# Kernel optimization log

Measured on AMD Instinct MI355X. Metric: run time of the kernel, lower is better.

The kernel has to match this reference:

```python
import jax, jax.numpy as jnp
import numpy as np

N_NODES = 100000
N_EDGES = 2000000
D_IN = 4
HID = 64


def setup_inputs() -> dict:
    key = jax.random.key(0)
    ks = jax.random.split(key, 8)
    node_feats = jax.random.normal(ks[0], (N_NODES, D_IN), dtype=jnp.float32)
    pairs = jax.random.randint(ks[1], (N_EDGES, 2), 0, N_NODES, dtype=jnp.int64)
    # Kaiming-ish init scaling
    W1 = jax.random.normal(ks[2], (D_IN, HID), dtype=jnp.float32) / np.sqrt(D_IN)
    b1 = jnp.zeros((HID,), dtype=jnp.float32)
    W2 = jax.random.normal(ks[3], (HID, HID), dtype=jnp.float32) / np.sqrt(HID)
    b2 = jnp.zeros((HID,), dtype=jnp.float32)
    We1 = jax.random.normal(ks[4], (3 * HID, HID), dtype=jnp.float32) / np.sqrt(3 * HID)
    be1 = jnp.zeros((HID,), dtype=jnp.float32)
    We2 = jax.random.normal(ks[5], (HID, 1), dtype=jnp.float32) / np.sqrt(HID)
    be2 = jnp.zeros((1,), dtype=jnp.float32)
    return {"node_feats": node_feats, "pairs": pairs, "W1": W1, "b1": b1,
            "W2": W2, "b2": b2, "We1": We1, "be1": be1, "We2": We2, "be2": be2}


def reference(node_feats, pairs, W1, b1, W2, b2, We1, be1, We2, be2):
    # node MLP: Linear -> ReLU -> Linear -> ReLU
    H = jax.nn.relu(node_feats @ W1 + b1)      # [N, HID]
    H = jax.nn.relu(H @ W2 + b2)               # [N, HID]
    # vectorized gather over all edge pairs (replaces Python loop)
    hu = H[pairs[:, 0]]                        # [E, HID]
    hv = H[pairs[:, 1]]                        # [E, HID]
    E = jnp.concatenate([hu, hv, jnp.abs(hu - hv)], axis=-1)  # [E, 3*HID]
    # edge MLP: Linear -> ReLU -> Linear, squeeze last dim
    scores = (jax.nn.relu(E @ We1 + be1) @ We2 + be2)[:, 0]   # [E]
    return scores
```

## Files before the change

### kernel.cpp

```cpp
#include <hip/hip_runtime.h>

#define N_NODES 100000
#define N_EDGES 2000000

typedef __bf16 bf16x8 __attribute__((ext_vector_type(8)));
typedef float f32x4 __attribute__((ext_vector_type(4)));

__device__ __forceinline__ unsigned f2bf_rne(float f) {
  unsigned u = __builtin_bit_cast(unsigned, f);
  u += 0x7FFFu + ((u >> 16) & 1u);
  return u >> 16;
}

__device__ __forceinline__ unsigned pack_rhu(float lo, float hi) {
  unsigned ulo = __builtin_bit_cast(unsigned, lo) + 0x8000u;
  unsigned uhi = __builtin_bit_cast(unsigned, hi) + 0x8000u;
  return __builtin_amdgcn_perm(uhi, ulo, 0x07060302u);
}

__device__ __forceinline__ unsigned absdiff_pack(unsigned a, unsigned b) {
  float alo = __builtin_bit_cast(float, a << 16);
  float ahi = __builtin_bit_cast(float, a & 0xFFFF0000u);
  float blo = __builtin_bit_cast(float, b << 16);
  float bhi = __builtin_bit_cast(float, b & 0xFFFF0000u);
  return pack_rhu(fabsf(alo - blo), fabsf(ahi - bhi));
}

__global__ __launch_bounds__(64, 1) void node_mfma_kernel(
    const float* __restrict__ X, const float* __restrict__ W1,
    const float* __restrict__ b1, const float* __restrict__ W2,
    const float* __restrict__ b2, unsigned short* __restrict__ H) {
  const int lane = threadIdx.x;
  const int l15 = lane & 15;
  const int quad = lane >> 4;

  float w1v[2][4][8], b1v[2][8];
#pragma unroll
  for (int c = 0; c < 2; ++c)
#pragma unroll
    for (int j = 0; j < 8; ++j) {
      int col = c * 32 + quad * 8 + j;
      b1v[c][j] = b1[col];
#pragma unroll
      for (int d = 0; d < 4; ++d) w1v[c][d][j] = W1[d * 64 + col];
    }

  uint4 afr[2][4];
#pragma unroll
  for (int c = 0; c < 2; ++c)
#pragma unroll
    for (int mt = 0; mt < 4; ++mt) {
      unsigned w[4];
#pragma unroll
      for (int p = 0; p < 4; ++p) {
        int k = c * 32 + quad * 8 + 2 * p;
        unsigned lo = f2bf_rne(W2[k * 64 + mt * 16 + l15]);
        unsigned hi = f2bf_rne(W2[(k + 1) * 64 + mt * 16 + l15]);
        w[p] = lo | (hi << 16);
      }
      afr[c][mt] = make_uint4(w[0], w[1], w[2], w[3]);
    }
  float b2v[16];
#pragma unroll
  for (int mt = 0; mt < 4; ++mt)
#pragma unroll
    for (int r = 0; r < 4; ++r) b2v[mt * 4 + r] = b2[mt * 16 + quad * 4 + r];

  const int ntiles = N_NODES / 16;
  for (int tile = blockIdx.x; tile < ntiles; tile += gridDim.x) {
    float4 xv = ((const float4*)X)[tile * 16 + l15];

    uint4 bfr[2];
#pragma unroll
    for (int c = 0; c < 2; ++c) {
      unsigned w[4];
#pragma unroll
      for (int p = 0; p < 4; ++p) {
        float h0 = fmaxf(b1v[c][2 * p] + xv.x * w1v[c][0][2 * p] +
                             xv.y * w1v[c][1][2 * p] + xv.z * w1v[c][2][2 * p] +
                             xv.w * w1v[c][3][2 * p],
                         0.f);
        float h1 = fmaxf(b1v[c][2 * p + 1] + xv.x * w1v[c][0][2 * p + 1] +
                             xv.y * w1v[c][1][2 * p + 1] +
                             xv.z * w1v[c][2][2 * p + 1] +
                             xv.w * w1v[c][3][2 * p + 1],
                         0.f);
        w[p] = pack_rhu(h0, h1);
      }
      bfr[c] = make_uint4(w[0], w[1], w[2], w[3]);
    }

    f32x4 acc[4];
#pragma unroll
    for (int mt = 0; mt < 4; ++mt) acc[mt] = (f32x4){0.f, 0.f, 0.f, 0.f};
#pragma unroll
    for (int c = 0; c < 2; ++c)
#pragma unroll
      for (int mt = 0; mt < 4; ++mt)
        acc[mt] = __builtin_amdgcn_mfma_f32_16x16x32_bf16(
            __builtin_bit_cast(bf16x8, afr[c][mt]),
            __builtin_bit_cast(bf16x8, bfr[c]), acc[mt], 0, 0, 0);

    unsigned short* hrow = H + (tile * 16 + l15) * 64;
#pragma unroll
    for (int mt = 0; mt < 4; ++mt) {
      unsigned lo = pack_rhu(fmaxf(acc[mt][0] + b2v[mt * 4 + 0], 0.f),
                             fmaxf(acc[mt][1] + b2v[mt * 4 + 1], 0.f));
      unsigned hi = pack_rhu(fmaxf(acc[mt][2] + b2v[mt * 4 + 2], 0.f),
                             fmaxf(acc[mt][3] + b2v[mt * 4 + 3], 0.f));
      *(uint2*)(hrow + mt * 16 + quad * 4) = make_uint2(lo, hi);
    }
  }
}

__global__ __launch_bounds__(256, 2) void edge_mlp_kernel(
    const unsigned short* __restrict__ H, const int* __restrict__ pairs,
    const float* __restrict__ We1, const float* __restrict__ be1,
    const float* __restrict__ We2, const float* __restrict__ be2,
    float* __restrict__ out) {
  const int tid = threadIdx.x;
  const int lane = tid & 63;
  const int l15 = lane & 15;
  const int quad = lane >> 4;

  uint4 afr[6][4];
#pragma unroll
  for (int c = 0; c < 6; ++c)
#pragma unroll
    for (int mt = 0; mt < 4; ++mt) {
      unsigned w[4];
#pragma unroll
      for (int p = 0; p < 4; ++p) {
        int k = c * 32 + quad * 8 + 2 * p;
        unsigned lo = f2bf_rne(We1[k * 64 + mt * 16 + l15]);
        unsigned hi = f2bf_rne(We1[(k + 1) * 64 + mt * 16 + l15]);
        w[p] = lo | (hi << 16);
      }
      afr[c][mt] = make_uint4(w[0], w[1], w[2], w[3]);
    }
  float be1v[16], we2v[16];
#pragma unroll
  for (int mt = 0; mt < 4; ++mt)
#pragma unroll
    for (int r = 0; r < 4; ++r) {
      be1v[mt * 4 + r] = be1[mt * 16 + quad * 4 + r];
      we2v[mt * 4 + r] = We2[mt * 16 + quad * 4 + r];
    }
  const float be2v = be2[0];

  const int wid = blockIdx.x * 4 + (tid >> 6);
  const int nw = gridDim.x * 4;
  const int ntiles = N_EDGES / 16;
  const int last = ntiles - 1;
  const int2* pairs2 = (const int2*)pairs;

  uint4 g[3][4];
  int2 uvn[3];
#pragma unroll
  for (int k = 0; k < 3; ++k) {
    int t = wid + k * nw;
    int2 uv = pairs2[(t <= last ? t : last) * 16 + l15];
    const uint4* pu = (const uint4*)(H + uv.x * 64 + quad * 8);
    const uint4* pv = (const uint4*)(H + uv.y * 64 + quad * 8);
    g[k][0] = pu[0];
    g[k][1] = pu[4];
    g[k][2] = pv[0];
    g[k][3] = pv[4];
    int tn = t + 3 * nw;
    uvn[k] = pairs2[(tn <= last ? tn : last) * 16 + l15];
  }

  for (int base = wid; base < ntiles; base += 3 * nw) {
#pragma unroll
    for (int k = 0; k < 3; ++k) {
      const int t = base + k * nw;

      uint4 ab0, ab1;
      ab0.x = absdiff_pack(g[k][0].x, g[k][2].x);
      ab0.y = absdiff_pack(g[k][0].y, g[k][2].y);
      ab0.z = absdiff_pack(g[k][0].z, g[k][2].z);
      ab0.w = absdiff_pack(g[k][0].w, g[k][2].w);
      ab1.x = absdiff_pack(g[k][1].x, g[k][3].x);
      ab1.y = absdiff_pack(g[k][1].y, g[k][3].y);
      ab1.z = absdiff_pack(g[k][1].z, g[k][3].z);
      ab1.w = absdiff_pack(g[k][1].w, g[k][3].w);

      bf16x8 b[6];
      b[0] = __builtin_bit_cast(bf16x8, g[k][0]);
      b[1] = __builtin_bit_cast(bf16x8, g[k][1]);
      b[2] = __builtin_bit_cast(bf16x8, g[k][2]);
      b[3] = __builtin_bit_cast(bf16x8, g[k][3]);
      b[4] = __builtin_bit_cast(bf16x8, ab0);
      b[5] = __builtin_bit_cast(bf16x8, ab1);

      f32x4 acc[4];
#pragma unroll
      for (int mt = 0; mt < 4; ++mt) acc[mt] = (f32x4){0.f, 0.f, 0.f, 0.f};
#pragma unroll
      for (int c = 0; c < 6; ++c)
#pragma unroll
        for (int mt = 0; mt < 4; ++mt)
          acc[mt] = __builtin_amdgcn_mfma_f32_16x16x32_bf16(
              __builtin_bit_cast(bf16x8, afr[c][mt]), b[c], acc[mt], 0, 0, 0);

      {
        const uint4* qu = (const uint4*)(H + uvn[k].x * 64 + quad * 8);
        const uint4* qv = (const uint4*)(H + uvn[k].y * 64 + quad * 8);
        g[k][0] = qu[0];
        g[k][1] = qu[4];
        g[k][2] = qv[0];
        g[k][3] = qv[4];
        int tn = t + 6 * nw;
        uvn[k] = pairs2[(tn <= last ? tn : last) * 16 + l15];
      }

      float s = 0.f;
#pragma unroll
      for (int mt = 0; mt < 4; ++mt)
#pragma unroll
        for (int r = 0; r < 4; ++r)
          s += fmaxf(acc[mt][r] + be1v[mt * 4 + r], 0.f) * we2v[mt * 4 + r];
      s += __shfl_xor(s, 16);
      s += __shfl_xor(s, 32);
      if (quad == 0 && t <= last) out[t * 16 + l15] = s + be2v;
    }
  }
}

extern "C" void kernel_launch(void* const* d_in, const int* in_sizes, int n_in,
                              void* d_out, int out_size, void* d_ws,
                              size_t ws_size, hipStream_t stream) {
  const float* X = (const float*)d_in[0];
  const int* pairs = (const int*)d_in[1];
  const float* W1 = (const float*)d_in[2];
  const float* b1 = (const float*)d_in[3];
  const float* W2 = (const float*)d_in[4];
  const float* b2 = (const float*)d_in[5];
  const float* We1 = (const float*)d_in[6];
  const float* be1 = (const float*)d_in[7];
  const float* We2 = (const float*)d_in[8];
  const float* be2 = (const float*)d_in[9];
  float* out = (float*)d_out;
  unsigned short* H = (unsigned short*)d_ws;

  node_mfma_kernel<<<1024, 64, 0, stream>>>(X, W1, b1, W2, b2, H);
  edge_mlp_kernel<<<1024, 256, 0, stream>>>(H, pairs, We1, be1, We2, be2, out);
}
```

Before: 168.6 us.

## Switch edge MLP to 32x32x16 MFMA with LDS-resident weights and bias folding

The edge kernel now processes 32 edges per wave tile using 32x32x16 bf16 MFMA instead of 16x16x32. The We1 weight fragments move from registers into shared memory and are read per MFMA. The be1 bias is folded into an extra K chunk paired with a constant-one operand. This is meant to cut MFMA instruction count and register pressure so more gathers stay in flight. In exchange it adds an LDS read per MFMA, does one extra MFMA chunk for the bias, and rounds the bias to bf16.

Measured after the change: 170.9 us. Within noise of the previous version (+1.4%).

```diff
diff --git a/kernel.cpp b/kernel.cpp
--- a/kernel.cpp
+++ b/kernel.cpp
@@ -5,6 +5,7 @@
 
 typedef __bf16 bf16x8 __attribute__((ext_vector_type(8)));
 typedef float f32x4 __attribute__((ext_vector_type(4)));
+typedef float f32x16 __attribute__((ext_vector_type(16)));
 
 __device__ __forceinline__ unsigned f2bf_rne(float f) {
   unsigned u = __builtin_bit_cast(unsigned, f);
@@ -118,111 +119,125 @@
     const float* __restrict__ We1, const float* __restrict__ be1,
     const float* __restrict__ We2, const float* __restrict__ be2,
     float* __restrict__ out) {
+  __shared__ uint4 wlds[26 * 64];
   const int tid = threadIdx.x;
+
+  for (int s = tid; s < 26 * 64; s += 256) {
+    int f = s >> 6, ln = s & 63;
+    int c = f >> 1, mt = f & 1;
+    int col = mt * 32 + (ln & 31);
+    uint4 val;
+    if (c < 12) {
+      int kb = c * 16 + (ln >> 5) * 8;
+      val.x = f2bf_rne(We1[(kb + 0) * 64 + col]) |
+              (f2bf_rne(We1[(kb + 1) * 64 + col]) << 16);
+      val.y = f2bf_rne(We1[(kb + 2) * 64 + col]) |
+              (f2bf_rne(We1[(kb + 3) * 64 + col]) << 16);
+      val.z = f2bf_rne(We1[(kb + 4) * 64 + col]) |
+              (f2bf_rne(We1[(kb + 5) * 64 + col]) << 16);
+      val.w = f2bf_rne(We1[(kb + 6) * 64 + col]) |
+              (f2bf_rne(We1[(kb + 7) * 64 + col]) << 16);
+    } else {
+      val.x = ((ln >> 5) == 0) ? f2bf_rne(be1[col]) : 0u;
+      val.y = 0u;
+      val.z = 0u;
+      val.w = 0u;
+    }
+    wlds[s] = val;
+  }
+
   const int lane = tid & 63;
-  const int l15 = lane & 15;
-  const int quad = lane >> 4;
-
-  uint4 afr[6][4];
-#pragma unroll
-  for (int c = 0; c < 6; ++c)
-#pragma unroll
-    for (int mt = 0; mt < 4; ++mt) {
-      unsigned w[4];
-#pragma unroll
-      for (int p = 0; p < 4; ++p) {
-        int k = c * 32 + quad * 8 + 2 * p;
-        unsigned lo = f2bf_rne(We1[k * 64 + mt * 16 + l15]);
-        unsigned hi = f2bf_rne(We1[(k + 1) * 64 + mt * 16 + l15]);
-        w[p] = lo | (hi << 16);
-      }
-      afr[c][mt] = make_uint4(w[0], w[1], w[2], w[3]);
-    }
-  float be1v[16], we2v[16];
-#pragma unroll
-  for (int mt = 0; mt < 4; ++mt)
-#pragma unroll
-    for (int r = 0; r < 4; ++r) {
-      be1v[mt * 4 + r] = be1[mt * 16 + quad * 4 + r];
-      we2v[mt * 4 + r] = We2[mt * 16 + quad * 4 + r];
-    }
+  const int n = lane & 31;
+  const int half = lane >> 5;
+
+  uint4 b13u = make_uint4((half == 0) ? 0x00003F80u : 0u, 0u, 0u, 0u);
+
+  float we2v[32];
+#pragma unroll
+  for (int mt = 0; mt < 2; ++mt)
+#pragma unroll
+    for (int r = 0; r < 16; ++r)
+      we2v[mt * 16 + r] = We2[mt * 32 + (r & 3) + 8 * (r >> 2) + 4 * half];
   const float be2v = be2[0];
+  __syncthreads();
 
   const int wid = blockIdx.x * 4 + (tid >> 6);
   const int nw = gridDim.x * 4;
-  const int ntiles = N_EDGES / 16;
+  const int ntiles = N_EDGES / 32;
   const int last = ntiles - 1;
   const int2* pairs2 = (const int2*)pairs;
-
-  uint4 g[3][4];
-  int2 uvn[3];
-#pragma unroll
-  for (int k = 0; k < 3; ++k) {
+  const uint4* wf = wlds + lane;
+
+  uint4 g[2][8];
+  int2 uvn[2];
+#pragma unroll
+  for (int k = 0; k < 2; ++k) {
     int t = wid + k * nw;
-    int2 uv = pairs2[(t <= last ? t : last) * 16 + l15];
-    const uint4* pu = (const uint4*)(H + uv.x * 64 + quad * 8);
-    const uint4* pv = (const uint4*)(H + uv.y * 64 + quad * 8);
-    g[k][0] = pu[0];
-    g[k][1] = pu[4];
-    g[k][2] = pv[0];
-    g[k][3] = pv[4];
-    int tn = t + 3 * nw;
-    uvn[k] = pairs2[(tn <= last ? tn : last) * 16 + l15];
-  }
-
-  for (int base = wid; base < ntiles; base += 3 * nw) {
-#pragma unroll
-    for (int k = 0; k < 3; ++k) {
-      const int t = base + k * nw;
-
-      uint4 ab0, ab1;
-      ab0.x = absdiff_pack(g[k][0].x, g[k][2].x);
-      ab0.y = absdiff_pack(g[k][0].y, g[k][2].y);
-      ab0.z = absdiff_pack(g[k][0].z, g[k][2].z);
-      ab0.w = absdiff_pack(g[k][0].w, g[k][2].w);
-      ab1.x = absdiff_pack(g[k][1].x, g[k][3].x);
-      ab1.y = absdiff_pack(g[k][1].y, g[k][3].y);
-      ab1.z = absdiff_pack(g[k][1].z, g[k][3].z);
-      ab1.w = absdiff_pack(g[k][1].w, g[k][3].w);
-
-      bf16x8 b[6];
-      b[0] = __builtin_bit_cast(bf16x8, g[k][0]);
-      b[1] = __builtin_bit_cast(bf16x8, g[k][1]);
-      b[2] = __builtin_bit_cast(bf16x8, g[k][2]);
-      b[3] = __builtin_bit_cast(bf16x8, g[k][3]);
-      b[4] = __builtin_bit_cast(bf16x8, ab0);
-      b[5] = __builtin_bit_cast(bf16x8, ab1);
-
-      f32x4 acc[4];
-#pragma unroll
-      for (int mt = 0; mt < 4; ++mt) acc[mt] = (f32x4){0.f, 0.f, 0.f, 0.f};
-#pragma unroll
-      for (int c = 0; c < 6; ++c)
-#pragma unroll
-        for (int mt = 0; mt < 4; ++mt)
-          acc[mt] = __builtin_amdgcn_mfma_f32_16x16x32_bf16(
-              __builtin_bit_cast(bf16x8, afr[c][mt]), b[c], acc[mt], 0, 0, 0);
+    t = (t <= last) ? t : last;
+    int2 uv = pairs2[t * 32 + n];
+    const uint4* pu = (const uint4*)(H + uv.x * 64 + half * 8);
+    const uint4* pv = (const uint4*)(H + uv.y * 64 + half * 8);
+#pragma unroll
+    for (int c = 0; c < 4; ++c) {
+      g[k][c] = pu[c * 2];
+      g[k][4 + c] = pv[c * 2];
+    }
+    int tn = wid + (k + 2) * nw;
+    tn = (tn <= last) ? tn : last;
+    uvn[k] = pairs2[tn * 32 + n];
+  }
+
+  for (int base = wid; base < ntiles; base += 2 * nw) {
+#pragma unroll
+    for (int k = 0; k < 2; ++k) {
+      int t = base + k * nw;
+      t = (t <= last) ? t : last;
+
+      uint4 ab[4];
+#pragma unroll
+      for (int c = 0; c < 4; ++c) {
+        ab[c].x = absdiff_pack(g[k][c].x, g[k][4 + c].x);
+        ab[c].y = absdiff_pack(g[k][c].y, g[k][4 + c].y);
+        ab[c].z = absdiff_pack(g[k][c].z, g[k][4 + c].z);
+        ab[c].w = absdiff_pack(g[k][c].w, g[k][4 + c].w);
+      }
+
+      f32x16 acc[2];
+      acc[0] = (f32x16)(0.f);
+      acc[1] = (f32x16)(0.f);
+#pragma unroll
+      for (int c = 0; c < 13; ++c) {
+        uint4 bu = (c < 8) ? g[k][c] : (c < 12 ? ab[c - 8] : b13u);
+        bf16x8 b = __builtin_bit_cast(bf16x8, bu);
+#pragma unroll
+        for (int mt = 0; mt < 2; ++mt) {
+          bf16x8 a = __builtin_bit_cast(bf16x8, wf[(c * 2 + mt) * 64]);
+          acc[mt] = __builtin_amdgcn_mfma_f32_32x32x16_bf16(a, b, acc[mt], 0,
+                                                            0, 0);
+        }
+      }
 
       {
-        const uint4* qu = (const uint4*)(H + uvn[k].x * 64 + quad * 8);
-        const uint4* qv = (const uint4*)(H + uvn[k].y * 64 + quad * 8);
-        g[k][0] = qu[0];
-        g[k][1] = qu[4];
-        g[k][2] = qv[0];
-        g[k][3] = qv[4];
-        int tn = t + 6 * nw;
-        uvn[k] = pairs2[(tn <= last ? tn : last) * 16 + l15];
+        const uint4* qu = (const uint4*)(H + uvn[k].x * 64 + half * 8);
+        const uint4* qv = (const uint4*)(H + uvn[k].y * 64 + half * 8);
+#pragma unroll
+        for (int c = 0; c < 4; ++c) {
+          g[k][c] = qu[c * 2];
+          g[k][4 + c] = qv[c * 2];
+        }
+        int tn = base + (k + 4) * nw;
+        tn = (tn <= last) ? tn : last;
+        uvn[k] = pairs2[tn * 32 + n];
       }
 
       float s = 0.f;
 #pragma unroll
-      for (int mt = 0; mt < 4; ++mt)
-#pragma unroll
-        for (int r = 0; r < 4; ++r)
-          s += fmaxf(acc[mt][r] + be1v[mt * 4 + r], 0.f) * we2v[mt * 4 + r];
-      s += __shfl_xor(s, 16);
+      for (int mt = 0; mt < 2; ++mt)
+#pragma unroll
+        for (int r = 0; r < 16; ++r)
+          s += fmaxf(acc[mt][r], 0.f) * we2v[mt * 16 + r];
       s += __shfl_xor(s, 32);
-      if (quad == 0 && t <= last) out[t * 16 + l15] = s + be2v;
+      if (half == 0) out[t * 32 + n] = s + be2v;
     }
   }
 }
```
